# Optimization experiments

Hardware: AMD Instinct MI355X
Metric: run time of the kernel (lower is better)

## Reference

```python
import jax, jax.numpy as jnp
import numpy as np

B, L, D = 8, 256, 32      # batch, key seq_len, input_dim
E, H, Q = 128, 8, 128     # embed_time, heads, num_query_steps
HID = 256                 # hidden_dim
V = 2 * D                 # value dim with mask channel
EK = E // H


def setup_inputs() -> dict:
    key = jax.random.key(0)
    ks = jax.random.split(key, 12)
    s = 0.05
    return {
        "values": jax.random.normal(ks[0], (B, L, D), jnp.float32),
        "mask": jax.random.randint(ks[1], (B, L, D), 0, 2).astype(jnp.int32),
        "times": jax.random.uniform(ks[2], (B, L), jnp.float32),
        # learn_time_embedding params (torch Linear(1, E-1) and Linear(1, 1))
        "w_per": jax.random.normal(ks[3], (1, E - 1), jnp.float32) * s,
        "b_per": jax.random.normal(ks[4], (E - 1,), jnp.float32) * s,
        "w_lin": jax.random.normal(ks[5], (1, 1), jnp.float32) * s,
        "b_lin": jax.random.normal(ks[6], (1,), jnp.float32) * s,
        # mTAND q/k linears (E,E) and output proj (HID, H*V)
        "wq": jax.random.normal(ks[7], (E, E), jnp.float32) * s,
        "bq": jnp.zeros((E,), jnp.float32),
        "wk": jax.random.normal(ks[8], (E, E), jnp.float32) * s,
        "bk": jnp.zeros((E,), jnp.float32),
        "wo": jax.random.normal(ks[9], (HID, H * V), jnp.float32) * s,
        "bo": jnp.zeros((HID,), jnp.float32),
        "ln_g": jnp.ones((HID,), jnp.float32),
        "ln_b": jnp.zeros((HID,), jnp.float32),
    }


def reference(values, mask, times, w_per, b_per, w_lin, b_lin,
              wq, bq, wk, bk, wo, bo, ln_g, ln_b):
    eps = 1e-6
    maskf = mask.astype(jnp.float32)                      # [B,L,D]
    obs = maskf.max(axis=-1) > 0                          # [B,L] observed steps
    # --- normalize times over observed steps ---
    tmin = jnp.where(obs, times, jnp.inf).min(axis=1, keepdims=True)
    tmax = jnp.where(obs, times, -jnp.inf).max(axis=1, keepdims=True)
    has = jnp.any(obs, axis=1, keepdims=True)             # [B,1]
    tmin = jnp.where(has, tmin, 0.0)
    tmax = jnp.where(has, tmax, 1.0)
    tn = (times - tmin) / jnp.maximum(tmax - tmin, eps)
    tn = jnp.where(obs, tn, 0.0)
    qt = jnp.broadcast_to(jnp.linspace(0.0, 1.0, Q, dtype=jnp.float32), (B, Q))

    def temb(tt):  # learnable time embedding: [linear(t), sin(periodic(t))]
        t = tt[..., None]                                 # [...,1]
        return jnp.concatenate([t @ w_lin.T + b_lin,
                                jnp.sin(t @ w_per + b_per)], axis=-1)

    tk = temb(tn)   # [B,L,E]
    tq = temb(qt)   # [B,Q,E]

    vinp = jnp.concatenate([values, maskf], axis=-1)      # [B,L,V]
    am = jnp.concatenate([maskf, maskf], axis=-1)         # [B,L,V]

    q = (tq @ wq.T + bq).reshape(B, Q, H, EK).transpose(0, 2, 1, 3)  # [B,H,Q,ek]
    k = (tk @ wk.T + bk).reshape(B, L, H, EK).transpose(0, 2, 1, 3)  # [B,H,L,ek]
    scores = jnp.einsum('bhqe,bhke->bhqk', q, k) / np.float32(np.sqrt(EK))
    # per-value-channel masked scores: [B,H,Q,L,V]
    s5 = jnp.where(am[:, None, None, :, :] == 0, jnp.float32(-10000.0),
                   scores[..., None])
    attn = jax.nn.softmax(s5, axis=-2)                    # softmax over L
    ctx = jnp.einsum('bhqkv,bkv->bhqv', attn, vinp)       # [B,H,Q,V]
    ctx = ctx.transpose(0, 2, 1, 3).reshape(B, Q, H * V)
    seq = ctx @ wo.T + bo                                 # [B,Q,HID]
    # LayerNorm (torch default eps=1e-5, biased var)
    mu = seq.mean(axis=-1, keepdims=True)
    var = ((seq - mu) ** 2).mean(axis=-1, keepdims=True)
    seq = (seq - mu) / jnp.sqrt(var + 1e-5) * ln_g + ln_b
    seq = seq * has.astype(jnp.float32)[:, :, None]       # zero seqs with no obs
    pooled = seq.mean(axis=1)
    return seq, pooled, qt
```

## Files before the change

### kernel.cpp

```cpp
#include <hip/hip_runtime.h>
#include <hip/hip_bf16.h>

#define B_   8
#define L_   256
#define D_   32
#define E_   128
#define H_   8
#define Q_   128
#define HID_ 256

__global__ __launch_bounds__(256) void k_prep1(
    const float* __restrict__ values, const int* __restrict__ mask,
    const float* __restrict__ times,
    const float* __restrict__ wo, const float* __restrict__ bo,
    float* __restrict__ tn, float* __restrict__ has,
    float* __restrict__ cm, float* __restrict__ colmean,
    float* __restrict__ mvm, unsigned* __restrict__ bitsT,
    float* __restrict__ qt_out, float* __restrict__ pooled,
    float* __restrict__ cvec)
{
    __shared__ float val_s[256][33];
    __shared__ float smin[256], smax[256];
    __shared__ unsigned bits_s[256];
    __shared__ float partial_s[8][32];
    __shared__ float cm_s[D_];
    __shared__ float sh[2];

    int b = blockIdx.x;
    int t = threadIdx.x;

    const int*   mrow = mask   + (size_t)(b * L_ + t) * D_;
    const float* vrow = values + (size_t)(b * L_ + t) * D_;
    int4  m4[8];
    float4 v4[8];
    int any = 0;
    #pragma unroll
    for (int j = 0; j < 8; ++j) {
        m4[j] = reinterpret_cast<const int4*>(mrow)[j];
        v4[j] = reinterpret_cast<const float4*>(vrow)[j];
        any |= m4[j].x | m4[j].y | m4[j].z | m4[j].w;
        float4 mv;
        mv.x = m4[j].x ? v4[j].x : 0.f;
        mv.y = m4[j].y ? v4[j].y : 0.f;
        mv.z = m4[j].z ? v4[j].z : 0.f;
        mv.w = m4[j].w ? v4[j].w : 0.f;
        reinterpret_cast<float4*>(mvm + (size_t)(b * L_ + t) * D_)[j] = mv;
        val_s[t][j * 4 + 0] = v4[j].x;
        val_s[t][j * 4 + 1] = v4[j].y;
        val_s[t][j * 4 + 2] = v4[j].z;
        val_s[t][j * 4 + 3] = v4[j].w;
    }
    int wave = t >> 6;
    #pragma unroll
    for (int d = 0; d < D_; ++d) {
        int comp;
        { int j = d >> 2, c = d & 3;
          int4 mm = m4[j];
          comp = (c == 0) ? mm.x : (c == 1) ? mm.y : (c == 2) ? mm.z : mm.w; }
        unsigned long long bal = __ballot(comp != 0);
        if ((t & 63) == 0) {
            bits_s[d * 8 + wave * 2 + 0] = (unsigned)(bal & 0xffffffffull);
            bits_s[d * 8 + wave * 2 + 1] = (unsigned)(bal >> 32);
        }
    }
    float tv = times[b * L_ + t];
    smin[t] = any ? tv : 1e38f;
    smax[t] = any ? tv : -1e38f;
    __syncthreads();
    for (int off = 128; off > 0; off >>= 1) {
        if (t < off) {
            smin[t] = fminf(smin[t], smin[t + off]);
            smax[t] = fmaxf(smax[t], smax[t + off]);
        }
        __syncthreads();
    }
    if (t == 0) {
        float mn = smin[0], mx = smax[0];
        float hv = (mn < 1e37f) ? 1.f : 0.f;
        sh[0] = (hv > 0.f) ? mn : 0.f;
        sh[1] = (hv > 0.f) ? mx : 1.f;
        has[b] = hv;
    }
    __syncthreads();
    float inv = 1.f / fmaxf(sh[1] - sh[0], 1e-6f);
    tn[b * L_ + t] = any ? (tv - sh[0]) * inv : 0.f;

    if (t < Q_) qt_out[b * Q_ + t] = (float)t * (1.f / 127.f);
    pooled[b * HID_ + t] = 0.f;
    bitsT[b * 256 + t] = bits_s[t];

    {
        int d = t & 31, lg = t >> 5;
        float ps = 0.f;
        #pragma unroll
        for (int i = 0; i < 32; ++i) ps += val_s[lg * 32 + i][d];
        partial_s[lg][d] = ps;
    }
    __syncthreads();
    if (t < D_) {
        float s = 0.f;
        #pragma unroll
        for (int lg = 0; lg < 8; ++lg) s += partial_s[lg][t];
        colmean[b * D_ + t] = s * (1.f / (float)L_);
        unsigned o = 0;
        #pragma unroll
        for (int w = 0; w < 8; ++w) o |= bits_s[t * 8 + w];
        float cmf = o ? 1.f : 0.f;
        cm[b * D_ + t] = cmf;
        cm_s[t] = cmf;
    }
    __syncthreads();

    {
        int hid = t;
        const float4* wrow4 = reinterpret_cast<const float4*>(wo + (size_t)hid * 512);
        float accm = 0.f;
        #pragma unroll
        for (int h1 = 0; h1 < 8; ++h1) {
            #pragma unroll
            for (int j = 0; j < 8; ++j) {
                float4 w = wrow4[h1 * 16 + 8 + j];
                accm += cm_s[j * 4 + 0] * w.x + cm_s[j * 4 + 1] * w.y
                      + cm_s[j * 4 + 2] * w.z + cm_s[j * 4 + 3] * w.w;
            }
        }
        cvec[b * HID_ + hid] = bo[hid] + accm;
    }
}

__global__ __launch_bounds__(256) void k_prep2(
    const float* __restrict__ tn,
    const float* __restrict__ w_per, const float* __restrict__ b_per,
    const float* __restrict__ w_lin, const float* __restrict__ b_lin,
    const float* __restrict__ wq, const float* __restrict__ bq,
    const float* __restrict__ wk, const float* __restrict__ bk,
    const float* __restrict__ wo,
    float* __restrict__ qproj, float* __restrict__ kproj,
    float* __restrict__ wotv)
{
    __shared__ __align__(16) float emb_q[2][E_];
    __shared__ __align__(16) float emb_k[8][E_];
    __shared__ float tsh[8];

    int blk = blockIdx.x;
    int t = threadIdx.x;

    if (blk < 64) {
        int half = t >> 7, e = t & 127;
        int q = blk * 2 + half;
        float tt = (float)q * (1.f / 127.f);
        emb_q[half][e] = (e == 0) ? (tt * w_lin[0] + b_lin[0])
                                  : __sinf(tt * w_per[e - 1] + b_per[e - 1]);
        __syncthreads();
        const float4* wr4 = reinterpret_cast<const float4*>(wq + (size_t)e * E_);
        const float4* e4  = reinterpret_cast<const float4*>(emb_q[half]);
        float acc = bq[e];
        #pragma unroll 8
        for (int j = 0; j < E_ / 4; ++j) {
            float4 w = wr4[j], x = e4[j];
            acc += w.x * x.x + w.y * x.y + w.z * x.z + w.w * x.w;
        }
        qproj[q * E_ + e] = acc;
    } else if (blk < 320) {
        int bl0 = (blk - 64) * 8;
        int e = t & 127, rh = t >> 7;
        if (t < 8) tsh[t] = tn[bl0 + t];
        __syncthreads();
        float wp = (e == 0) ? 0.f : w_per[e - 1];
        float bp = (e == 0) ? 0.f : b_per[e - 1];
        float wl = w_lin[0], bl = b_lin[0];
        #pragma unroll
        for (int rr = 0; rr < 4; ++rr) {
            int r = rh * 4 + rr;
            float tt = tsh[r];
            emb_k[r][e] = (e == 0) ? (tt * wl + bl) : __sinf(tt * wp + bp);
        }
        __syncthreads();
        const float4* wr4 = reinterpret_cast<const float4*>(wk + (size_t)e * E_);
        float bias = bk[e];
        float acc[4] = {bias, bias, bias, bias};
        #pragma unroll 8
        for (int j = 0; j < E_ / 4; ++j) {
            float4 w = wr4[j];
            #pragma unroll
            for (int rr = 0; rr < 4; ++rr) {
                float4 x = *reinterpret_cast<const float4*>(&emb_k[rh * 4 + rr][j * 4]);
                acc[rr] += w.x * x.x + w.y * x.y + w.z * x.z + w.w * x.w;
            }
        }
        #pragma unroll
        for (int rr = 0; rr < 4; ++rr)
            kproj[(size_t)(bl0 + rh * 4 + rr) * E_ + e] = acc[rr];
    } else {
        int c0 = (blk - 320) * 4;
        #pragma unroll
        for (int j = 0; j < 4; ++j) {
            int c = c0 + j;
            int col = (c >> 5) * 64 + (c & 31);
            wotv[(size_t)c * HID_ + t] = wo[(size_t)t * 512 + col];
        }
    }
}

__global__ __launch_bounds__(256, 3) void k_main(
    const float* __restrict__ qproj, const float* __restrict__ kproj,
    const float* __restrict__ mvm, const unsigned* __restrict__ bitsT,
    const float* __restrict__ cm, const float* __restrict__ colmean,
    const float* __restrict__ wotv, const float* __restrict__ cvec,
    const float* __restrict__ has,
    const float* __restrict__ ln_g, const float* __restrict__ ln_b,
    float* __restrict__ seq_out, float* __restrict__ pooled)
{
    int q = blockIdx.x, b = blockIdx.y;
    int tid = threadIdx.x;
    __shared__ __align__(16) float mvm_s[L_ * D_];
    __shared__ __align__(16) float e_s[L_ * H_];
    __shared__ __align__(16) float qv_s[E_];
    __shared__ unsigned bits_s[256];
    __shared__ float gmax_s[H_];
    __shared__ __align__(16) float ctx_s[256];
    __shared__ float red_s[8];
    __shared__ float mu_rs[2];

    {
        const float4* src = reinterpret_cast<const float4*>(mvm + (size_t)b * L_ * D_);
        float4* dst = reinterpret_cast<float4*>(mvm_s);
        #pragma unroll
        for (int j = 0; j < 8; ++j) dst[tid + j * 256] = src[tid + j * 256];
        bits_s[tid] = bitsT[b * 256 + tid];
        if (tid < E_) qv_s[tid] = qproj[q * E_ + tid];
    }
    __syncthreads();

    const float4* kr4 = reinterpret_cast<const float4*>(kproj + (size_t)(b * L_ + tid) * E_);
    const float4* qv4 = reinterpret_cast<const float4*>(qv_s);
    float s[H_];
    #pragma unroll
    for (int h = 0; h < H_; ++h) {
        float acc = 0.f;
        #pragma unroll
        for (int j = 0; j < 4; ++j) {
            float4 kk = kr4[h * 4 + j], qq = qv4[h * 4 + j];
            acc += kk.x * qq.x + kk.y * qq.y + kk.z * qq.z + kk.w * qq.w;
        }
        s[h] = acc * 0.25f;
    }
    {
        float4* er4 = reinterpret_cast<float4*>(e_s + tid * 8);
        er4[0] = *reinterpret_cast<float4*>(&s[0]);
        er4[1] = *reinterpret_cast<float4*>(&s[4]);
    }
    __syncthreads();
    {
        int h = tid >> 5, ln = tid & 31;
        float mx = -1e30f;
        #pragma unroll
        for (int j = 0; j < 8; ++j) mx = fmaxf(mx, e_s[(ln + j * 32) * 8 + h]);
        #pragma unroll
        for (int off = 16; off > 0; off >>= 1) mx = fmaxf(mx, __shfl_xor(mx, off));
        if (ln == 0) gmax_s[h] = mx;
    }
    __syncthreads();
    {
        float e8[H_];
        #pragma unroll
        for (int h = 0; h < H_; ++h) e8[h] = __expf(s[h] - gmax_s[h]);
        float4* er4 = reinterpret_cast<float4*>(e_s + tid * 8);
        er4[0] = *reinterpret_cast<float4*>(&e8[0]);
        er4[1] = *reinterpret_cast<float4*>(&e8[4]);
    }
    __syncthreads();

    {
        int lseg = tid >> 6, h = (tid >> 3) & 7, d4 = tid & 7;
        unsigned w0[4], w1[4];
        #pragma unroll
        for (int j = 0; j < 4; ++j) {
            int d = d4 * 4 + j;
            w0[j] = bits_s[d * 8 + lseg * 2 + 0];
            w1[j] = bits_s[d * 8 + lseg * 2 + 1];
        }
        float4 av  = {0.f, 0.f, 0.f, 0.f};
        float4 den = {0.f, 0.f, 0.f, 0.f};
        const float4* mv4 = reinterpret_cast<const float4*>(mvm_s);
        int l0 = lseg * 64;
        #pragma unroll 8
        for (int i = 0; i < 32; ++i) {
            int l = l0 + i;
            float e = e_s[l * 8 + h];
            float4 m = mv4[l * 8 + d4];
            av.x += e * m.x; av.y += e * m.y; av.z += e * m.z; av.w += e * m.w;
            den.x += ((w0[0] >> i) & 1u) ? e : 0.f;
            den.y += ((w0[1] >> i) & 1u) ? e : 0.f;
            den.z += ((w0[2] >> i) & 1u) ? e : 0.f;
            den.w += ((w0[3] >> i) & 1u) ? e : 0.f;
        }
        #pragma unroll 8
        for (int i = 0; i < 32; ++i) {
            int l = l0 + 32 + i;
            float e = e_s[l * 8 + h];
            float4 m = mv4[l * 8 + d4];
            av.x += e * m.x; av.y += e * m.y; av.z += e * m.z; av.w += e * m.w;
            den.x += ((w1[0] >> i) & 1u) ? e : 0.f;
            den.y += ((w1[1] >> i) & 1u) ? e : 0.f;
            den.z += ((w1[2] >> i) & 1u) ? e : 0.f;
            den.w += ((w1[3] >> i) & 1u) ? e : 0.f;
        }
        __syncthreads();
        float4* p4 = reinterpret_cast<float4*>(mvm_s);
        p4[tid * 2 + 0] = av;
        p4[tid * 2 + 1] = den;
    }
    __syncthreads();
    {
        const float* part = mvm_s;
        int hh = tid >> 5, dd = tid & 31, dg = dd >> 2, jj = dd & 3;
        float a = 0.f, dn = 0.f;
        #pragma unroll
        for (int ls = 0; ls < 4; ++ls) {
            int pt = ls * 64 + hh * 8 + dg;
            a  += part[pt * 8 + jj];
            dn += part[pt * 8 + 4 + jj];
        }
        float cmf = cm[b * D_ + dd];
        ctx_s[tid] = (cmf > 0.f) ? (a / dn) : colmean[b * D_ + dd];
    }
    __syncthreads();

    int hid = tid;
    float acc = cvec[b * HID_ + hid];
    #pragma unroll 4
    for (int c4 = 0; c4 < 64; ++c4) {
        float w0 = wotv[(size_t)(c4 * 4 + 0) * HID_ + hid];
        float w1 = wotv[(size_t)(c4 * 4 + 1) * HID_ + hid];
        float w2 = wotv[(size_t)(c4 * 4 + 2) * HID_ + hid];
        float w3 = wotv[(size_t)(c4 * 4 + 3) * HID_ + hid];
        float4 cx = *reinterpret_cast<const float4*>(&ctx_s[c4 * 4]);
        acc += cx.x * w0 + cx.y * w1 + cx.z * w2 + cx.w * w3;
    }

    int wave = hid >> 6;
    {
        float sum = acc, ssum = acc * acc;
        #pragma unroll
        for (int off = 32; off > 0; off >>= 1) {
            sum  += __shfl_xor(sum, off);
            ssum += __shfl_xor(ssum, off);
        }
        if ((hid & 63) == 0) { red_s[wave] = sum; red_s[4 + wave] = ssum; }
    }
    __syncthreads();
    if (hid == 0) {
        float S  = red_s[0] + red_s[1] + red_s[2] + red_s[3];
        float SS = red_s[4] + red_s[5] + red_s[6] + red_s[7];
        float mu = S * (1.f / HID_);
        float var = SS * (1.f / HID_) - mu * mu;
        mu_rs[0] = mu;
        mu_rs[1] = rsqrtf(var + 1e-5f);
    }
    __syncthreads();

    float outv = ((acc - mu_rs[0]) * mu_rs[1] * ln_g[hid] + ln_b[hid]) * has[b];
    seq_out[((size_t)(b * Q_ + q)) * HID_ + hid] = outv;
    atomicAdd(&pooled[b * HID_ + hid], outv * (1.f / (float)Q_));
}

extern "C" void kernel_launch(void* const* d_in, const int* in_sizes, int n_in,
                              void* d_out, int out_size, void* d_ws, size_t ws_size,
                              hipStream_t stream)
{
    const float* values = (const float*)d_in[0];
    const int*   mask   = (const int*)  d_in[1];
    const float* times  = (const float*)d_in[2];
    const float* w_per  = (const float*)d_in[3];
    const float* b_per  = (const float*)d_in[4];
    const float* w_lin  = (const float*)d_in[5];
    const float* b_lin  = (const float*)d_in[6];
    const float* wq     = (const float*)d_in[7];
    const float* bq     = (const float*)d_in[8];
    const float* wk     = (const float*)d_in[9];
    const float* bk     = (const float*)d_in[10];
    const float* wo     = (const float*)d_in[11];
    const float* bo     = (const float*)d_in[12];
    const float* ln_g   = (const float*)d_in[13];
    const float* ln_b   = (const float*)d_in[14];

    float* out     = (float*)d_out;
    float* seq_out = out;
    float* pooled  = out + 262144;
    float* qt_out  = out + 262144 + 2048;

    float* ws         = (float*)d_ws;
    float*    tn      = ws;
    float*    has     = ws + 2048;
    float*    cm      = ws + 2056;
    float*    colmean = ws + 2312;
    float*    qproj   = ws + 2568;
    unsigned* bitsT   = (unsigned*)(ws + 18952);
    float*    mvm     = ws + 21000;
    float*    kproj   = ws + 86536;
    float*    cvec    = ws + 348680;
    float*    wotv    = ws + 350728;

    k_prep1<<<B_,            256, 0, stream>>>(values, mask, times, wo, bo,
                 tn, has, cm, colmean, mvm, bitsT, qt_out, pooled, cvec);
    k_prep2<<<384,           256, 0, stream>>>(tn, w_per, b_per, w_lin, b_lin,
                 wq, bq, wk, bk, wo, qproj, kproj, wotv);
    k_main <<<dim3(Q_, B_),  256, 0, stream>>>(qproj, kproj, mvm, bitsT,
                 cm, colmean, wotv, cvec, has, ln_g, ln_b, seq_out, pooled);
}
```

Measured before the change: 148.1 us.

## Process two query steps per main block and move cvec computation to prep2

The main kernel now handles two query positions per block, so the kproj row, the mvm tile, the mask bits and the wotv weights each load once and serve two queries. This halves the grid and the redundant per-block loads and atomics. Separately, the cvec projection moves out of the 8-block prep1 into 8 extra prep2 blocks, and the min/max reduction in prep1 uses wave shuffles instead of a shared-memory tree. In exchange the main kernel uses more registers and shared memory per block, which may lower occupancy, and the grid shrinks to 512 blocks.

```diff
diff --git a/kernel.cpp b/kernel.cpp
--- a/kernel.cpp
+++ b/kernel.cpp
@@ -12,18 +12,15 @@
 __global__ __launch_bounds__(256) void k_prep1(
     const float* __restrict__ values, const int* __restrict__ mask,
     const float* __restrict__ times,
-    const float* __restrict__ wo, const float* __restrict__ bo,
     float* __restrict__ tn, float* __restrict__ has,
     float* __restrict__ cm, float* __restrict__ colmean,
     float* __restrict__ mvm, unsigned* __restrict__ bitsT,
-    float* __restrict__ qt_out, float* __restrict__ pooled,
-    float* __restrict__ cvec)
+    float* __restrict__ qt_out, float* __restrict__ pooled)
 {
     __shared__ float val_s[256][33];
-    __shared__ float smin[256], smax[256];
     __shared__ unsigned bits_s[256];
     __shared__ float partial_s[8][32];
-    __shared__ float cm_s[D_];
+    __shared__ float sminw[4], smaxw[4];
     __shared__ float sh[2];
 
     int b = blockIdx.x;
@@ -64,18 +61,27 @@
         }
     }
     float tv = times[b * L_ + t];
-    smin[t] = any ? tv : 1e38f;
-    smax[t] = any ? tv : -1e38f;
-    __syncthreads();
-    for (int off = 128; off > 0; off >>= 1) {
-        if (t < off) {
-            smin[t] = fminf(smin[t], smin[t + off]);
-            smax[t] = fmaxf(smax[t], smax[t + off]);
-        }
-        __syncthreads();
-    }
+    {
+        float wmin = any ? tv : 1e38f;
+        float wmax = any ? tv : -1e38f;
+        #pragma unroll
+        for (int off = 32; off > 0; off >>= 1) {
+            wmin = fminf(wmin, __shfl_xor(wmin, off));
+            wmax = fmaxf(wmax, __shfl_xor(wmax, off));
+        }
+        if ((t & 63) == 0) { sminw[wave] = wmin; smaxw[wave] = wmax; }
+    }
+    {
+        int d = t & 31, lg = t >> 5;
+        float ps = 0.f;
+        #pragma unroll
+        for (int i = 0; i < 32; ++i) ps += val_s[lg * 32 + i][d];
+        partial_s[lg][d] = ps;
+    }
+    __syncthreads();
     if (t == 0) {
-        float mn = smin[0], mx = smax[0];
+        float mn = fminf(fminf(sminw[0], sminw[1]), fminf(sminw[2], sminw[3]));
+        float mx = fmaxf(fmaxf(smaxw[0], smaxw[1]), fmaxf(smaxw[2], smaxw[3]));
         float hv = (mn < 1e37f) ? 1.f : 0.f;
         sh[0] = (hv > 0.f) ? mn : 0.f;
         sh[1] = (hv > 0.f) ? mx : 1.f;
@@ -89,14 +95,6 @@
     pooled[b * HID_ + t] = 0.f;
     bitsT[b * 256 + t] = bits_s[t];
 
-    {
-        int d = t & 31, lg = t >> 5;
-        float ps = 0.f;
-        #pragma unroll
-        for (int i = 0; i < 32; ++i) ps += val_s[lg * 32 + i][d];
-        partial_s[lg][d] = ps;
-    }
-    __syncthreads();
     if (t < D_) {
         float s = 0.f;
         #pragma unroll
@@ -105,42 +103,24 @@
         unsigned o = 0;
         #pragma unroll
         for (int w = 0; w < 8; ++w) o |= bits_s[t * 8 + w];
-        float cmf = o ? 1.f : 0.f;
-        cm[b * D_ + t] = cmf;
-        cm_s[t] = cmf;
-    }
-    __syncthreads();
-
-    {
-        int hid = t;
-        const float4* wrow4 = reinterpret_cast<const float4*>(wo + (size_t)hid * 512);
-        float accm = 0.f;
-        #pragma unroll
-        for (int h1 = 0; h1 < 8; ++h1) {
-            #pragma unroll
-            for (int j = 0; j < 8; ++j) {
-                float4 w = wrow4[h1 * 16 + 8 + j];
-                accm += cm_s[j * 4 + 0] * w.x + cm_s[j * 4 + 1] * w.y
-                      + cm_s[j * 4 + 2] * w.z + cm_s[j * 4 + 3] * w.w;
-            }
-        }
-        cvec[b * HID_ + hid] = bo[hid] + accm;
+        cm[b * D_ + t] = o ? 1.f : 0.f;
     }
 }
 
 __global__ __launch_bounds__(256) void k_prep2(
-    const float* __restrict__ tn,
+    const float* __restrict__ tn, const float* __restrict__ cm,
     const float* __restrict__ w_per, const float* __restrict__ b_per,
     const float* __restrict__ w_lin, const float* __restrict__ b_lin,
     const float* __restrict__ wq, const float* __restrict__ bq,
     const float* __restrict__ wk, const float* __restrict__ bk,
-    const float* __restrict__ wo,
+    const float* __restrict__ wo, const float* __restrict__ bo,
     float* __restrict__ qproj, float* __restrict__ kproj,
-    float* __restrict__ wotv)
+    float* __restrict__ wotv, float* __restrict__ cvec)
 {
     __shared__ __align__(16) float emb_q[2][E_];
     __shared__ __align__(16) float emb_k[8][E_];
     __shared__ float tsh[8];
+    __shared__ float cm_s[D_];
 
     int blk = blockIdx.x;
     int t = threadIdx.x;
@@ -191,7 +171,7 @@
         #pragma unroll
         for (int rr = 0; rr < 4; ++rr)
             kproj[(size_t)(bl0 + rh * 4 + rr) * E_ + e] = acc[rr];
-    } else {
+    } else if (blk < 384) {
         int c0 = (blk - 320) * 4;
         #pragma unroll
         for (int j = 0; j < 4; ++j) {
@@ -199,6 +179,23 @@
             int col = (c >> 5) * 64 + (c & 31);
             wotv[(size_t)c * HID_ + t] = wo[(size_t)t * 512 + col];
         }
+    } else {
+        int b = blk - 384;
+        if (t < D_) cm_s[t] = cm[b * D_ + t];
+        __syncthreads();
+        int hid = t;
+        const float4* wrow4 = reinterpret_cast<const float4*>(wo + (size_t)hid * 512);
+        float accm = 0.f;
+        #pragma unroll
+        for (int h1 = 0; h1 < 8; ++h1) {
+            #pragma unroll
+            for (int j = 0; j < 8; ++j) {
+                float4 w = wrow4[h1 * 16 + 8 + j];
+                accm += cm_s[j * 4 + 0] * w.x + cm_s[j * 4 + 1] * w.y
+                      + cm_s[j * 4 + 2] * w.z + cm_s[j * 4 + 3] * w.w;
+            }
+        }
+        cvec[b * HID_ + hid] = bo[hid] + accm;
     }
 }
 
@@ -211,16 +208,16 @@
     const float* __restrict__ ln_g, const float* __restrict__ ln_b,
     float* __restrict__ seq_out, float* __restrict__ pooled)
 {
-    int q = blockIdx.x, b = blockIdx.y;
+    int qb = blockIdx.x, b = blockIdx.y;
     int tid = threadIdx.x;
     __shared__ __align__(16) float mvm_s[L_ * D_];
-    __shared__ __align__(16) float e_s[L_ * H_];
-    __shared__ __align__(16) float qv_s[E_];
+    __shared__ __align__(16) float e_s[2][L_ * H_];
+    __shared__ __align__(16) float qv_s[2][E_];
     __shared__ unsigned bits_s[256];
-    __shared__ float gmax_s[H_];
-    __shared__ __align__(16) float ctx_s[256];
-    __shared__ float red_s[8];
-    __shared__ float mu_rs[2];
+    __shared__ float gmax_s[16];
+    __shared__ __align__(16) float ctx_s[2][256];
+    __shared__ float red_s[2][8];
+    __shared__ float mu_rs[2][2];
 
     {
         const float4* src = reinterpret_cast<const float4*>(mvm + (size_t)b * L_ * D_);
@@ -228,46 +225,61 @@
         #pragma unroll
         for (int j = 0; j < 8; ++j) dst[tid + j * 256] = src[tid + j * 256];
         bits_s[tid] = bitsT[b * 256 + tid];
-        if (tid < E_) qv_s[tid] = qproj[q * E_ + tid];
+        int half = tid >> 7, e = tid & 127;
+        qv_s[half][e] = qproj[(qb * 2 + half) * E_ + e];
     }
     __syncthreads();
 
     const float4* kr4 = reinterpret_cast<const float4*>(kproj + (size_t)(b * L_ + tid) * E_);
-    const float4* qv4 = reinterpret_cast<const float4*>(qv_s);
-    float s[H_];
+    const float4* q04 = reinterpret_cast<const float4*>(qv_s[0]);
+    const float4* q14 = reinterpret_cast<const float4*>(qv_s[1]);
+    float s0[H_], s1[H_];
     #pragma unroll
     for (int h = 0; h < H_; ++h) {
-        float acc = 0.f;
+        float a0 = 0.f, a1 = 0.f;
         #pragma unroll
         for (int j = 0; j < 4; ++j) {
-            float4 kk = kr4[h * 4 + j], qq = qv4[h * 4 + j];
-            acc += kk.x * qq.x + kk.y * qq.y + kk.z * qq.z + kk.w * qq.w;
-        }
-        s[h] = acc * 0.25f;
-    }
-    {
-        float4* er4 = reinterpret_cast<float4*>(e_s + tid * 8);
-        er4[0] = *reinterpret_cast<float4*>(&s[0]);
-        er4[1] = *reinterpret_cast<float4*>(&s[4]);
-    }
-    __syncthreads();
-    {
-        int h = tid >> 5, ln = tid & 31;
+            float4 kk = kr4[h * 4 + j];
+            float4 qa = q04[h * 4 + j], qb4 = q14[h * 4 + j];
+            a0 += kk.x * qa.x + kk.y * qa.y + kk.z * qa.z + kk.w * qa.w;
+            a1 += kk.x * qb4.x + kk.y * qb4.y + kk.z * qb4.z + kk.w * qb4.w;
+        }
+        s0[h] = a0 * 0.25f;
+        s1[h] = a1 * 0.25f;
+    }
+    {
+        float4* e04 = reinterpret_cast<float4*>(&e_s[0][tid * 8]);
+        float4* e14 = reinterpret_cast<float4*>(&e_s[1][tid * 8]);
+        e04[0] = *reinterpret_cast<float4*>(&s0[0]);
+        e04[1] = *reinterpret_cast<float4*>(&s0[4]);
+        e14[0] = *reinterpret_cast<float4*>(&s1[0]);
+        e14[1] = *reinterpret_cast<float4*>(&s1[4]);
+    }
+    __syncthreads();
+    {
+        int g = tid >> 4, ln = tid & 15;
+        int qi = g >> 3, h = g & 7;
         float mx = -1e30f;
         #pragma unroll
-        for (int j = 0; j < 8; ++j) mx = fmaxf(mx, e_s[(ln + j * 32) * 8 + h]);
-        #pragma unroll
-        for (int off = 16; off > 0; off >>= 1) mx = fmaxf(mx, __shfl_xor(mx, off));
-        if (ln == 0) gmax_s[h] = mx;
-    }
-    __syncthreads();
-    {
-        float e8[H_];
-        #pragma unroll
-        for (int h = 0; h < H_; ++h) e8[h] = __expf(s[h] - gmax_s[h]);
-        float4* er4 = reinterpret_cast<float4*>(e_s + tid * 8);
-        er4[0] = *reinterpret_cast<float4*>(&e8[0]);
-        er4[1] = *reinterpret_cast<float4*>(&e8[4]);
+        for (int j = 0; j < 16; ++j) mx = fmaxf(mx, e_s[qi][(ln + j * 16) * 8 + h]);
+        #pragma unroll
+        for (int off = 8; off > 0; off >>= 1) mx = fmaxf(mx, __shfl_xor(mx, off));
+        if (ln == 0) gmax_s[g] = mx;
+    }
+    __syncthreads();
+    {
+        float e0[H_], e1[H_];
+        #pragma unroll
+        for (int h = 0; h < H_; ++h) {
+            e0[h] = __expf(s0[h] - gmax_s[h]);
+            e1[h] = __expf(s1[h] - gmax_s[8 + h]);
+        }
+        float4* e04 = reinterpret_cast<float4*>(&e_s[0][tid * 8]);
+        float4* e14 = reinterpret_cast<float4*>(&e_s[1][tid * 8]);
+        e04[0] = *reinterpret_cast<float4*>(&e0[0]);
+        e04[1] = *reinterpret_cast<float4*>(&e0[4]);
+        e14[0] = *reinterpret_cast<float4*>(&e1[0]);
+        e14[1] = *reinterpret_cast<float4*>(&e1[4]);
     }
     __syncthreads();
 
@@ -280,89 +292,114 @@
             w0[j] = bits_s[d * 8 + lseg * 2 + 0];
             w1[j] = bits_s[d * 8 + lseg * 2 + 1];
         }
-        float4 av  = {0.f, 0.f, 0.f, 0.f};
-        float4 den = {0.f, 0.f, 0.f, 0.f};
+        float4 av0 = {0,0,0,0}, dn0 = {0,0,0,0};
+        float4 av1 = {0,0,0,0}, dn1 = {0,0,0,0};
         const float4* mv4 = reinterpret_cast<const float4*>(mvm_s);
+        const float* e0p = e_s[0];
+        const float* e1p = e_s[1];
         int l0 = lseg * 64;
         #pragma unroll 8
         for (int i = 0; i < 32; ++i) {
             int l = l0 + i;
-            float e = e_s[l * 8 + h];
+            float ea = e0p[l * 8 + h], eb = e1p[l * 8 + h];
             float4 m = mv4[l * 8 + d4];
-            av.x += e * m.x; av.y += e * m.y; av.z += e * m.z; av.w += e * m.w;
-            den.x += ((w0[0] >> i) & 1u) ? e : 0.f;
-            den.y += ((w0[1] >> i) & 1u) ? e : 0.f;
-            den.z += ((w0[2] >> i) & 1u) ? e : 0.f;
-            den.w += ((w0[3] >> i) & 1u) ? e : 0.f;
+            av0.x += ea * m.x; av0.y += ea * m.y; av0.z += ea * m.z; av0.w += ea * m.w;
+            av1.x += eb * m.x; av1.y += eb * m.y; av1.z += eb * m.z; av1.w += eb * m.w;
+            bool b0 = (w0[0] >> i) & 1u, b1 = (w0[1] >> i) & 1u;
+            bool b2 = (w0[2] >> i) & 1u, b3 = (w0[3] >> i) & 1u;
+            dn0.x += b0 ? ea : 0.f; dn1.x += b0 ? eb : 0.f;
+            dn0.y += b1 ? ea : 0.f; dn1.y += b1 ? eb : 0.f;
+            dn0.z += b2 ? ea : 0.f; dn1.z += b2 ? eb : 0.f;
+            dn0.w += b3 ? ea : 0.f; dn1.w += b3 ? eb : 0.f;
         }
         #pragma unroll 8
         for (int i = 0; i < 32; ++i) {
             int l = l0 + 32 + i;
-            float e = e_s[l * 8 + h];
+            float ea = e0p[l * 8 + h], eb = e1p[l * 8 + h];
             float4 m = mv4[l * 8 + d4];
-            av.x += e * m.x; av.y += e * m.y; av.z += e * m.z; av.w += e * m.w;
-            den.x += ((w1[0] >> i) & 1u) ? e : 0.f;
-            den.y += ((w1[1] >> i) & 1u) ? e : 0.f;
-            den.z += ((w1[2] >> i) & 1u) ? e : 0.f;
-            den.w += ((w1[3] >> i) & 1u) ? e : 0.f;
+            av0.x += ea * m.x; av0.y += ea * m.y; av0.z += ea * m.z; av0.w += ea * m.w;
+            av1.x += eb * m.x; av1.y += eb * m.y; av1.z += eb * m.z; av1.w += eb * m.w;
+            bool b0 = (w1[0] >> i) & 1u, b1 = (w1[1] >> i) & 1u;
+            bool b2 = (w1[2] >> i) & 1u, b3 = (w1[3] >> i) & 1u;
+            dn0.x += b0 ? ea : 0.f; dn1.x += b0 ? eb : 0.f;
+            dn0.y += b1 ? ea : 0.f; dn1.y += b1 ? eb : 0.f;
+            dn0.z += b2 ? ea : 0.f; dn1.z += b2 ? eb : 0.f;
+            dn0.w += b3 ? ea : 0.f; dn1.w += b3 ? eb : 0.f;
         }
         __syncthreads();
         float4* p4 = reinterpret_cast<float4*>(mvm_s);
-        p4[tid * 2 + 0] = av;
-        p4[tid * 2 + 1] = den;
-    }
-    __syncthreads();
-    {
-        const float* part = mvm_s;
+        p4[tid * 4 + 0] = av0;
+        p4[tid * 4 + 1] = dn0;
+        p4[tid * 4 + 2] = av1;
+        p4[tid * 4 + 3] = dn1;
+    }
+    __syncthreads();
+    {
         int hh = tid >> 5, dd = tid & 31, dg = dd >> 2, jj = dd & 3;
-        float a = 0.f, dn = 0.f;
+        float a0 = 0.f, d0 = 0.f, a1 = 0.f, d1 = 0.f;
         #pragma unroll
         for (int ls = 0; ls < 4; ++ls) {
             int pt = ls * 64 + hh * 8 + dg;
-            a  += part[pt * 8 + jj];
-            dn += part[pt * 8 + 4 + jj];
+            a0 += mvm_s[pt * 16 + jj];
+            d0 += mvm_s[pt * 16 + 4 + jj];
+            a1 += mvm_s[pt * 16 + 8 + jj];
+            d1 += mvm_s[pt * 16 + 12 + jj];
         }
         float cmf = cm[b * D_ + dd];
-        ctx_s[tid] = (cmf > 0.f) ? (a / dn) : colmean[b * D_ + dd];
+        float cmn = colmean[b * D_ + dd];
+        ctx_s[0][tid] = (cmf > 0.f) ? (a0 / d0) : cmn;
+        ctx_s[1][tid] = (cmf > 0.f) ? (a1 / d1) : cmn;
     }
     __syncthreads();
 
     int hid = tid;
-    float acc = cvec[b * HID_ + hid];
+    float cv = cvec[b * HID_ + hid];
+    float acc0 = cv, acc1 = cv;
     #pragma unroll 4
     for (int c4 = 0; c4 < 64; ++c4) {
         float w0 = wotv[(size_t)(c4 * 4 + 0) * HID_ + hid];
         float w1 = wotv[(size_t)(c4 * 4 + 1) * HID_ + hid];
         float w2 = wotv[(size_t)(c4 * 4 + 2) * HID_ + hid];
         float w3 = wotv[(size_t)(c4 * 4 + 3) * HID_ + hid];
-        float4 cx = *reinterpret_cast<const float4*>(&ctx_s[c4 * 4]);
-        acc += cx.x * w0 + cx.y * w1 + cx.z * w2 + cx.w * w3;
+        float4 c0 = *reinterpret_cast<const float4*>(&ctx_s[0][c4 * 4]);
+        float4 c1 = *reinterpret_cast<const float4*>(&ctx_s[1][c4 * 4]);
+        acc0 += c0.x * w0 + c0.y * w1 + c0.z * w2 + c0.w * w3;
+        acc1 += c1.x * w0 + c1.y * w1 + c1.z * w2 + c1.w * w3;
     }
 
     int wave = hid >> 6;
     {
-        float sum = acc, ssum = acc * acc;
+        float su0 = acc0, ss0 = acc0 * acc0;
+        float su1 = acc1, ss1 = acc1 * acc1;
         #pragma unroll
         for (int off = 32; off > 0; off >>= 1) {
-            sum  += __shfl_xor(sum, off);
-            ssum += __shfl_xor(ssum, off);
-        }
-        if ((hid & 63) == 0) { red_s[wave] = sum; red_s[4 + wave] = ssum; }
-    }
-    __syncthreads();
-    if (hid == 0) {
-        float S  = red_s[0] + red_s[1] + red_s[2] + red_s[3];
-        float SS = red_s[4] + red_s[5] + red_s[6] + red_s[7];
+            su0 += __shfl_xor(su0, off);
+            ss0 += __shfl_xor(ss0, off);
+            su1 += __shfl_xor(su1, off);
+            ss1 += __shfl_xor(ss1, off);
+        }
+        if ((hid & 63) == 0) {
+            red_s[0][wave] = su0; red_s[0][4 + wave] = ss0;
+            red_s[1][wave] = su1; red_s[1][4 + wave] = ss1;
+        }
+    }
+    __syncthreads();
+    if (hid < 2) {
+        float S  = red_s[hid][0] + red_s[hid][1] + red_s[hid][2] + red_s[hid][3];
+        float SS = red_s[hid][4] + red_s[hid][5] + red_s[hid][6] + red_s[hid][7];
         float mu = S * (1.f / HID_);
         float var = SS * (1.f / HID_) - mu * mu;
-        mu_rs[0] = mu;
-        mu_rs[1] = rsqrtf(var + 1e-5f);
-    }
-    __syncthreads();
-
-    float outv = ((acc - mu_rs[0]) * mu_rs[1] * ln_g[hid] + ln_b[hid]) * has[b];
-    seq_out[((size_t)(b * Q_ + q)) * HID_ + hid] = outv;
-    atomicAdd(&pooled[b * HID_ + hid], outv * (1.f / (float)Q_));
+        mu_rs[hid][0] = mu;
+        mu_rs[hid][1] = rsqrtf(var + 1e-5f);
+    }
+    __syncthreads();
+
+    float g = ln_g[hid], bb = ln_b[hid], hasb = has[b];
+    float out0 = ((acc0 - mu_rs[0][0]) * mu_rs[0][1] * g + bb) * hasb;
+    float out1 = ((acc1 - mu_rs[1][0]) * mu_rs[1][1] * g + bb) * hasb;
+    seq_out[((size_t)(b * Q_ + qb * 2 + 0)) * HID_ + hid] = out0;
+    seq_out[((size_t)(b * Q_ + qb * 2 + 1)) * HID_ + hid] = out1;
+    atomicAdd(&pooled[b * HID_ + hid], (out0 + out1) * (1.f / (float)Q_));
 }
 
 extern "C" void kernel_launch(void* const* d_in, const int* in_sizes, int n_in,
@@ -402,10 +439,10 @@
     float*    cvec    = ws + 348680;
     float*    wotv    = ws + 350728;
 
-    k_prep1<<<B_,            256, 0, stream>>>(values, mask, times, wo, bo,
-                 tn, has, cm, colmean, mvm, bitsT, qt_out, pooled, cvec);
-    k_prep2<<<384,           256, 0, stream>>>(tn, w_per, b_per, w_lin, b_lin,
-                 wq, bq, wk, bk, wo, qproj, kproj, wotv);
-    k_main <<<dim3(Q_, B_),  256, 0, stream>>>(qproj, kproj, mvm, bitsT,
+    k_prep1<<<B_,               256, 0, stream>>>(values, mask, times,
+                 tn, has, cm, colmean, mvm, bitsT, qt_out, pooled);
+    k_prep2<<<392,              256, 0, stream>>>(tn, cm, w_per, b_per, w_lin, b_lin,
+                 wq, bq, wk, bk, wo, bo, qproj, kproj, wotv, cvec);
+    k_main <<<dim3(Q_ / 2, B_), 256, 0, stream>>>(qproj, kproj, mvm, bitsT,
                  cm, colmean, wotv, cvec, has, ln_g, ln_b, seq_out, pooled);
 }
```

Result: faster. 133.6 us (-9.8%).
